# Optimization experiments

Hardware: AMD Instinct MI355X
Metric: run time of the kernel (lower is better)

## Reference

```python
import jax, jax.numpy as jnp
import numpy as np

MAX_TOP_K = 3
NUM_EXPERTS = 64
B, S, D = 4, 4096, 4096
H = D // 2


def setup_inputs() -> dict:
    key = jax.random.key(0)
    k0, k1, k2, k3 = jax.random.split(key, 4)
    x = jax.random.normal(k0, (B, S, D), dtype=jnp.float32)
    W = jax.random.normal(k1, (D, NUM_EXPERTS), dtype=jnp.float32) * 0.1
    # top_k_predictor: Linear(D, D//2) -> ReLU -> Linear(D//2, 1) -> Sigmoid
    W1 = jax.random.normal(k2, (D, H), dtype=jnp.float32) * (1.0 / np.sqrt(D))
    b1 = jnp.zeros((H,), dtype=jnp.float32)
    W2 = jax.random.normal(k3, (H, 1), dtype=jnp.float32) * (1.0 / np.sqrt(H))
    b2 = jnp.zeros((1,), dtype=jnp.float32)
    return {"x": x, "W": W, "W1": W1, "b1": b1, "W2": W2, "b2": b2}


def reference(x, W, W1, b1, W2, b2):
    b, s, d = x.shape
    x_flat = x.reshape(-1, d)                                  # [N, D]
    n = x_flat.shape[0]

    # small predictor MLP -> per-token dynamic k
    h = jax.nn.relu(x_flat @ W1 + b1)                          # [N, H]
    top_k_scores = jax.nn.sigmoid(h @ W2 + b2)[:, 0]           # [N]
    dynamic_top_k = jnp.clip(
        jnp.round(top_k_scores * MAX_TOP_K) + 1.0, 1.0, float(MAX_TOP_K)
    ).astype(jnp.int32)                                        # [N]

    # gating matmul + softmax + top-k
    gate_probs = jax.nn.softmax(x_flat @ W, axis=-1)           # [N, E]
    top_k_probs, top_k_indices = jax.lax.top_k(gate_probs, MAX_TOP_K)  # [N, K]

    # per-token dynamic-k mask and renormalize
    k_mask = jnp.arange(MAX_TOP_K)[None, :] < dynamic_top_k[:, None]   # [N, K]
    top_k_probs = top_k_probs * k_mask.astype(top_k_probs.dtype)
    top_k_weights = top_k_probs / (top_k_probs.sum(-1, keepdims=True) + 1e-8)

    # routing mask: 1 where expert is in top-k AND its (masked) weight > 0
    rows = jnp.arange(n)[:, None]                              # [N, 1]
    routing_mask = jnp.zeros((n, NUM_EXPERTS), top_k_weights.dtype).at[
        rows, top_k_indices
    ].set((top_k_weights > 0).astype(top_k_weights.dtype))     # [N, E]

    return (
        top_k_weights,
        top_k_indices,
        routing_mask.reshape(b, s, NUM_EXPERTS),
        dynamic_top_k,
    )
```

## Files before the change

### kernel.cpp

```cpp
#include <hip/hip_runtime.h>
#include <hip/hip_bf16.h>
#include <math.h>

#define DD   4096
#define HH   2048
#define NE   64
#define BK   32
#define NT   16
#define GM   32

typedef __attribute__((ext_vector_type(8))) short bf16x8;
typedef __attribute__((ext_vector_type(4))) float f32x4;

__device__ __forceinline__ void async16(void* lds, const void* g) {
    __builtin_amdgcn_global_load_lds(
        (const __attribute__((address_space(1))) unsigned int*)g,
        (__attribute__((address_space(3))) unsigned int*)lds, 16, 0, 0);
}

__device__ __forceinline__ void split2(float a, float b, unsigned& hi, unsigned& lo) {
    __hip_bfloat162 h = __float22bfloat162_rn(make_float2(a, b));
    float2 hf = __bfloat1622float2(h);
    __hip_bfloat162 l = __float22bfloat162_rn(make_float2(a - hf.x, b - hf.y));
    __builtin_memcpy(&hi, &h, 4);
    __builtin_memcpy(&lo, &l, 4);
}

__global__ __launch_bounds__(256) void split_xf(
    const float* __restrict__ x, uint4* __restrict__ xfh, uint4* __restrict__ xfl)
{
    const int t = threadIdx.x;
    const int mt = blockIdx.x >> 7;
    const int ks = blockIdx.x & 127;
#pragma unroll
    for (int s2 = 0; s2 < 2; ++s2) {
        int s = t + s2 * 256;
        int fb = s >> 6, ln = s & 63;
        int row = mt * 128 + fb * 16 + (ln & 15);
        int k   = ks * 32 + (ln >> 4) * 8;
        const float* g = x + (size_t)row * DD + k;
        float4 a = *(const float4*)g, b = *(const float4*)(g + 4);
        unsigned h0, l0, h1, l1, h2, l2, h3, l3;
        split2(a.x, a.y, h0, l0); split2(a.z, a.w, h1, l1);
        split2(b.x, b.y, h2, l2); split2(b.z, b.w, h3, l3);
        size_t idx = ((size_t)blockIdx.x * 8 + fb) * 64 + ln;
        xfh[idx] = make_uint4(h0, h1, h2, h3);
        xfl[idx] = make_uint4(l0, l1, l2, l3);
    }
}

__global__ __launch_bounds__(256) void split_w1t(
    const float* __restrict__ W1,
    unsigned short* __restrict__ th, unsigned short* __restrict__ tl)
{
    __shared__ float ts[32][33];
    const int n0 = blockIdx.x * 32, k0 = blockIdx.y * 32;
    const int t = threadIdx.x;
    {
        int r = t >> 3, c4 = (t & 7) * 4;
        float4 v = *(const float4*)&W1[(size_t)(k0 + r) * HH + n0 + c4];
        ts[r][c4] = v.x; ts[r][c4 + 1] = v.y; ts[r][c4 + 2] = v.z; ts[r][c4 + 3] = v.w;
    }
    __syncthreads();
    int n = t >> 3, kk = (t & 7) * 4;
    float f0 = ts[kk][n], f1 = ts[kk + 1][n], f2 = ts[kk + 2][n], f3 = ts[kk + 3][n];
    unsigned h0, l0, h1, l1;
    split2(f0, f1, h0, l0); split2(f2, f3, h1, l1);
    *(uint2*)&th[(size_t)(n0 + n) * DD + k0 + kk] = make_uint2(h0, h1);
    *(uint2*)&tl[(size_t)(n0 + n) * DD + k0 + kk] = make_uint2(l0, l1);
}

template<bool PRE_A>
__global__ __launch_bounds__(256, 3) void pred_mfma(
    const float* __restrict__ x,
    const unsigned short* __restrict__ xh, const unsigned short* __restrict__ xl,
    const unsigned short* __restrict__ w1th, const unsigned short* __restrict__ w1tl,
    const float* __restrict__ b1, const float* __restrict__ W2,
    double* __restrict__ pl)
{
    __shared__ __align__(16) char lds[32768];

    const int t = threadIdx.x, wv = t >> 6, ln = t & 63;
    const int lin = blockIdx.x;
    const int sub = lin >> 3;
    const int ntile = (lin & 7) * 2 + (sub & 1);
    const int mtile = sub >> 1;
    const int m0 = mtile * 128, n0 = ntile * 128;
    const int frow = ln & 15;
    const int fkb  = (ln >> 4) * 8;

    f32x4 acc[4][4];
#pragma unroll
    for (int i = 0; i < 4; ++i)
#pragma unroll
        for (int j = 0; j < 4; ++j) acc[i][j] = (f32x4){0.f, 0.f, 0.f, 0.f};

    const int mb = (wv & 1) * 4, nb = (wv >> 1) * 4;

    if (PRE_A) {
        const unsigned short* bsrc = (wv & 2) ? w1tl : w1th;
        const int roleoff = ((wv & 2) ? 8192 : 0) + (wv & 1) * 4096;
        const unsigned short* bg =
            bsrc + (size_t)(n0 + (wv & 1) * 64 + frow) * DD + fkb;

        const uint4* gh = (const uint4*)xh + ((size_t)mtile * 1024 + mb) * 64 + ln;
        const uint4* gl = (const uint4*)xl + ((size_t)mtile * 1024 + mb) * 64 + ln;

        bf16x8 ah[4], al[4];

#pragma unroll
        for (int q = 0; q < 4; ++q)
            async16(lds + roleoff + q * 1024, bg + (size_t)q * 16 * DD);
        __builtin_amdgcn_sched_barrier(0);
#pragma unroll
        for (int i = 0; i < 4; ++i) {
            ah[i] = *(const bf16x8*)(gh + i * 64);
            al[i] = *(const bf16x8*)(gl + i * 64);
        }
        asm volatile("s_waitcnt vmcnt(8)" ::: "memory");
        __builtin_amdgcn_s_barrier();

        for (int ks = 0; ks < 128; ++ks) {
            const int rb = (ks & 1) << 14;
            const int sb = rb ^ 16384;
            const bool more = (ks + 1 < 128);

            if (more) {
#pragma unroll
                for (int q = 0; q < 4; ++q)
                    async16(lds + sb + roleoff + q * 1024,
                            bg + (size_t)q * 16 * DD + (ks + 1) * BK);
            }
            __builtin_amdgcn_sched_barrier(0);

            bf16x8 bfh[4], bfl[4];
#pragma unroll
            for (int j = 0; j < 4; ++j) {
                bfh[j] = *(const bf16x8*)(lds + rb + (nb + j) * 1024 + ln * 16);
                bfl[j] = *(const bf16x8*)(lds + rb + 8192 + (nb + j) * 1024 + ln * 16);
            }

#pragma unroll
            for (int i = 0; i < 4; ++i)
#pragma unroll
                for (int j = 0; j < 4; ++j) {
                    acc[i][j] = __builtin_amdgcn_mfma_f32_16x16x32_bf16(ah[i], bfh[j], acc[i][j], 0, 0, 0);
                    acc[i][j] = __builtin_amdgcn_mfma_f32_16x16x32_bf16(ah[i], bfl[j], acc[i][j], 0, 0, 0);
                }
            if (more) {
#pragma unroll
                for (int i = 0; i < 4; ++i)
                    ah[i] = *(const bf16x8*)(gh + (size_t)(ks + 1) * 512 + i * 64);
            }
#pragma unroll
            for (int i = 0; i < 4; ++i)
#pragma unroll
                for (int j = 0; j < 4; ++j)
                    acc[i][j] = __builtin_amdgcn_mfma_f32_16x16x32_bf16(al[i], bfh[j], acc[i][j], 0, 0, 0);
            if (more) {
#pragma unroll
                for (int i = 0; i < 4; ++i)
                    al[i] = *(const bf16x8*)(gl + (size_t)(ks + 1) * 512 + i * 64);
                asm volatile("s_waitcnt vmcnt(8)" ::: "memory");
                __builtin_amdgcn_s_barrier();
            }
        }
    } else {
        char* Ah = lds;
        char* Al = lds + 8192;
        char* Bh = lds + 16384;
        char* Bl = lds + 24576;
        const unsigned short* gBh = w1th + (size_t)(n0 + frow) * DD + fkb;
        const unsigned short* gBl = w1tl + (size_t)(n0 + frow) * DD + fkb;

        for (int kc = 0; kc < DD; kc += BK) {
#pragma unroll
            for (int q = 0; q < 2; ++q) {
                int fb = wv * 2 + q;
                async16(Bh + fb * 1024, gBh + (size_t)fb * 16 * DD + kc);
                async16(Bl + fb * 1024, gBl + (size_t)fb * 16 * DD + kc);
            }
#pragma unroll
            for (int s2 = 0; s2 < 2; ++s2) {
                int s = t + s2 * 256;
                int fb = s >> 6, sl = s & 63;
                int row = fb * 16 + (sl & 15), kb = (sl >> 4) * 8;
                const float* g = x + (size_t)(m0 + row) * DD + kc + kb;
                float4 a = *(const float4*)g, b = *(const float4*)(g + 4);
                unsigned h0, l0, h1, l1, h2, l2, h3, l3;
                split2(a.x, a.y, h0, l0); split2(a.z, a.w, h1, l1);
                split2(b.x, b.y, h2, l2); split2(b.z, b.w, h3, l3);
                *(uint4*)(Ah + s * 16) = make_uint4(h0, h1, h2, h3);
                *(uint4*)(Al + s * 16) = make_uint4(l0, l1, l2, l3);
            }
            __syncthreads();

            bf16x8 afh[4], afl[4], bfh[4], bfl[4];
#pragma unroll
            for (int i = 0; i < 4; ++i) {
                afh[i] = *(const bf16x8*)(Ah + (mb + i) * 1024 + ln * 16);
                afl[i] = *(const bf16x8*)(Al + (mb + i) * 1024 + ln * 16);
                bfh[i] = *(const bf16x8*)(Bh + (nb + i) * 1024 + ln * 16);
                bfl[i] = *(const bf16x8*)(Bl + (nb + i) * 1024 + ln * 16);
            }
#pragma unroll
            for (int i = 0; i < 4; ++i)
#pragma unroll
                for (int j = 0; j < 4; ++j) {
                    acc[i][j] = __builtin_amdgcn_mfma_f32_16x16x32_bf16(afh[i], bfh[j], acc[i][j], 0, 0, 0);
                    acc[i][j] = __builtin_amdgcn_mfma_f32_16x16x32_bf16(afh[i], bfl[j], acc[i][j], 0, 0, 0);
                    acc[i][j] = __builtin_amdgcn_mfma_f32_16x16x32_bf16(afl[i], bfh[j], acc[i][j], 0, 0, 0);
                }
            __syncthreads();
        }
    }

    __syncthreads();
    double* redd = (double*)lds;
    const int mh = wv & 1, nh = wv >> 1;
    float b1v[4], w2v[4];
#pragma unroll
    for (int j = 0; j < 4; ++j) {
        int col = n0 + nh * 64 + j * 16 + frow;
        b1v[j] = b1[col];
        w2v[j] = W2[col];
    }
#pragma unroll
    for (int i = 0; i < 4; ++i)
#pragma unroll
        for (int r = 0; r < 4; ++r) {
            double s = 0.0;
#pragma unroll
            for (int j = 0; j < 4; ++j) {
                float h = acc[i][j][r] + b1v[j];
                h = fmaxf(h, 0.f);
                s += (double)h * (double)w2v[j];
            }
#pragma unroll
            for (int o = 1; o < 16; o <<= 1) s += __shfl_xor(s, o, 64);
            if (frow == 0)
                redd[nh * 128 + mh * 64 + i * 16 + (ln >> 4) * 4 + r] = s;
        }
    __syncthreads();
    if (t < 128)
        pl[(size_t)(m0 + t) * NT + ntile] = redd[t] + redd[128 + t];
}

__global__ __launch_bounds__(256) void pred_gemm(
    const float* __restrict__ x, const float* __restrict__ W1,
    const float* __restrict__ b1, const float* __restrict__ W2,
    double* __restrict__ pl)
{
    __shared__ float As[BK][128];
    __shared__ float Bs[BK][128];
    __shared__ double red[128][NT + 1];

    const int ht = blockIdx.x;
    const int tm = blockIdx.y;
    const int t  = threadIdx.x;
    const int tx = t & 15, ty = t >> 4;
    const int h0 = ht * 128;
    const int m0 = tm * 128;

    float acc[8][8];
#pragma unroll
    for (int i = 0; i < 8; ++i)
#pragma unroll
        for (int j = 0; j < 8; ++j) acc[i][j] = 0.f;

    const int arow = t >> 1, acol = (t & 1) << 4;
    const int brow = t >> 3, bcol = (t & 7) << 4;
    const float* xrow = x  + (size_t)(m0 + arow) * DD + acol;
    const float* wrow = W1 + (size_t)brow * HH + h0 + bcol;

    for (int k0 = 0; k0 < DD; k0 += BK) {
        float4 a4[4], b4[4];
        const float4* ap = (const float4*)(xrow + k0);
#pragma unroll
        for (int i = 0; i < 4; ++i) a4[i] = ap[i];
        const float4* bp = (const float4*)(wrow + (size_t)k0 * HH);
#pragma unroll
        for (int i = 0; i < 4; ++i) b4[i] = bp[i];
        __syncthreads();
#pragma unroll
        for (int i = 0; i < 4; ++i) {
            As[acol + i * 4 + 0][arow] = a4[i].x;
            As[acol + i * 4 + 1][arow] = a4[i].y;
            As[acol + i * 4 + 2][arow] = a4[i].z;
            As[acol + i * 4 + 3][arow] = a4[i].w;
        }
#pragma unroll
        for (int i = 0; i < 4; ++i)
            *(float4*)&Bs[brow][bcol + i * 4] = b4[i];
        __syncthreads();
#pragma unroll 8
        for (int kk = 0; kk < BK; ++kk) {
            float4 a0  = *(const float4*)&As[kk][ty * 8];
            float4 a1  = *(const float4*)&As[kk][ty * 8 + 4];
            float4 bb0 = *(const float4*)&Bs[kk][tx * 8];
            float4 bb1 = *(const float4*)&Bs[kk][tx * 8 + 4];
            float av[8] = {a0.x, a0.y, a0.z, a0.w, a1.x, a1.y, a1.z, a1.w};
            float bv[8] = {bb0.x, bb0.y, bb0.z, bb0.w, bb1.x, bb1.y, bb1.z, bb1.w};
#pragma unroll
            for (int i = 0; i < 8; ++i)
#pragma unroll
                for (int j = 0; j < 8; ++j)
                    acc[i][j] = fmaf(av[i], bv[j], acc[i][j]);
        }
    }
    __syncthreads();
#pragma unroll
    for (int r = 0; r < 8; ++r) {
        double s = 0.0;
#pragma unroll
        for (int c = 0; c < 8; ++c) {
            int h = h0 + tx * 8 + c;
            float v = acc[r][c] + b1[h];
            v = v > 0.f ? v : 0.f;
            s += (double)v * (double)W2[h];
        }
        red[ty * 8 + r][tx] = s;
    }
    __syncthreads();
    if (t < 128) {
        double s = 0.0;
#pragma unroll
        for (int j = 0; j < NT; ++j) s += red[t][j];
        pl[(size_t)(m0 + t) * NT + ht] = s;
    }
}

__global__ __launch_bounds__(256) void gate_fused(
    const float* __restrict__ x, const float* __restrict__ W,
    const double* __restrict__ pl, const float* __restrict__ b2,
    float* __restrict__ out, int Ntok)
{
    __shared__ __align__(16) char smem[GM * (NE + 1) * sizeof(double)];
    float (*As)[GM] = (float(*)[GM])smem;
    float (*Bs)[NE] = (float(*)[NE])(smem + BK * GM * 4);
    double (*Dm)[NE + 1] = (double(*)[NE + 1])smem;

    const int tm = blockIdx.x;
    const int t  = threadIdx.x;
    const int tx = t & 15, ty = t >> 4;
    const int m0 = tm * GM;

    double acc[2][4];
#pragma unroll
    for (int i = 0; i < 2; ++i)
#pragma unroll
        for (int j = 0; j < 4; ++j) acc[i][j] = 0.0;

    const int arow = t >> 3, acol = (t & 7) * 4;
    const int brow = t >> 3, bcol = (t & 7) * 8;
    const float* xrow = x + (size_t)(m0 + arow) * DD + acol;
    const float* wrow = W + (size_t)brow * NE + bcol;

    float4 a4  = *(const float4*)xrow;
    float4 b40 = *(const float4*)wrow;
    float4 b41 = *(const float4*)(wrow + 4);

    for (int k0 = 0; k0 < DD; k0 += BK) {
        __syncthreads();
        As[acol + 0][arow] = a4.x;
        As[acol + 1][arow] = a4.y;
        As[acol + 2][arow] = a4.z;
        As[acol + 3][arow] = a4.w;
        *(float4*)&Bs[brow][bcol]     = b40;
        *(float4*)&Bs[brow][bcol + 4] = b41;
        __syncthreads();

        if (k0 + BK < DD) {
            a4  = *(const float4*)(xrow + k0 + BK);
            b40 = *(const float4*)(wrow + (size_t)(k0 + BK) * NE);
            b41 = *(const float4*)(wrow + (size_t)(k0 + BK) * NE + 4);
        }

#pragma unroll 8
        for (int kk = 0; kk < BK; ++kk) {
            double a0 = (double)As[kk][ty * 2];
            double a1 = (double)As[kk][ty * 2 + 1];
            float4 b = *(const float4*)&Bs[kk][tx * 4];
            double bv[4] = {(double)b.x, (double)b.y, (double)b.z, (double)b.w};
#pragma unroll
            for (int j = 0; j < 4; ++j) {
                acc[0][j] = fma(a0, bv[j], acc[0][j]);
                acc[1][j] = fma(a1, bv[j], acc[1][j]);
            }
        }
    }

    __syncthreads();
#pragma unroll
    for (int r = 0; r < 2; ++r)
#pragma unroll
        for (int c = 0; c < 4; ++c)
            Dm[ty * 2 + r][tx * 4 + c] = acc[r][c];
    __syncthreads();

    const int wave = t >> 6;
    const int lane = t & 63;
    const double b2v = (double)b2[0];

    for (int i = 0; i < 8; ++i) {
        const int tl = wave * 8 + i;
        const int token = m0 + tl;
        double g = Dm[tl][lane];

        double mx = g;
#pragma unroll
        for (int o = 32; o > 0; o >>= 1) mx = fmax(mx, __shfl_xor(mx, o, 64));
        double e = exp(g - mx);
        double s = e;
#pragma unroll
        for (int o = 32; o > 0; o >>= 1) s += __shfl_xor(s, o, 64);
        double p = e / s;

        double pv = p; int pi = lane;
        double vt[3]; int it[3];
#pragma unroll
        for (int j = 0; j < 3; ++j) {
            double v = pv; int idx = pi;
#pragma unroll
            for (int o = 32; o > 0; o >>= 1) {
                double ov = __shfl_xor(v, o, 64);
                int    oi = __shfl_xor(idx, o, 64);
                if (ov > v || (ov == v && oi < idx)) { v = ov; idx = oi; }
            }
            vt[j] = v; it[j] = idx;
            if (lane == idx) pv = -1.0;
        }

        double plv = (lane < NT) ? pl[(size_t)token * NT + lane] : 0.0;
#pragma unroll
        for (int o = 32; o > 0; o >>= 1) plv += __shfl_xor(plv, o, 64);
        double logit = plv + b2v;
        double score = 1.0 / (1.0 + exp(-logit));
        int k = (int)rint(score * 3.0) + 1;
        k = k < 1 ? 1 : (k > 3 ? 3 : k);

        double wmask[3]; double wsum = 0.0;
#pragma unroll
        for (int j = 0; j < 3; ++j) { wmask[j] = (j < k) ? vt[j] : 0.0; wsum += wmask[j]; }
        double denom = wsum + 1e-8;
        float wn[3];
#pragma unroll
        for (int j = 0; j < 3; ++j) wn[j] = (float)(wmask[j] / denom);

        float mval = 0.f;
#pragma unroll
        for (int j = 0; j < 3; ++j)
            if (it[j] == lane && wn[j] > 0.f) mval = 1.f;

        out[(size_t)6 * Ntok + (size_t)token * NE + lane] = mval;
        if (lane < 3) {
            out[(size_t)token * 3 + lane] = wn[lane];
            out[(size_t)3 * Ntok + (size_t)token * 3 + lane] = (float)it[lane];
        }
        if (lane == 0) out[(size_t)70 * Ntok + token] = (float)k;
    }
}

extern "C" void kernel_launch(void* const* d_in, const int* in_sizes, int n_in,
                              void* d_out, int out_size, void* d_ws, size_t ws_size,
                              hipStream_t stream)
{
    const float* x  = (const float*)d_in[0];
    const float* W  = (const float*)d_in[1];
    const float* W1 = (const float*)d_in[2];
    const float* b1 = (const float*)d_in[3];
    const float* W2 = (const float*)d_in[4];
    const float* b2 = (const float*)d_in[5];
    float* out = (float*)d_out;

    const int Ntok = in_sizes[0] / DD;

    double* pl = (double*)d_ws;
    const size_t pl_b   = (size_t)Ntok * NT * sizeof(double);
    const size_t o_w1h  = (pl_b + 255) & ~(size_t)255;
    const size_t w1_b   = (size_t)DD * HH * 2;
    const size_t o_w1l  = o_w1h + w1_b;
    const size_t o_xh   = o_w1l + w1_b;
    const size_t x_b    = (size_t)Ntok * DD * 2;
    const size_t o_xl   = o_xh + x_b;
    const size_t need_w1   = o_xh;
    const size_t need_full = o_xl + x_b;

    const bool ok128 = (Ntok % 128) == 0;

    if (ok128 && ws_size >= need_w1) {
        unsigned short* w1th = (unsigned short*)((char*)d_ws + o_w1h);
        unsigned short* w1tl = (unsigned short*)((char*)d_ws + o_w1l);
        split_w1t<<<dim3(HH / 32, DD / 32), 256, 0, stream>>>(W1, w1th, w1tl);
        if (ws_size >= need_full) {
            unsigned short* xfh = (unsigned short*)((char*)d_ws + o_xh);
            unsigned short* xfl = (unsigned short*)((char*)d_ws + o_xl);
            split_xf<<<Ntok, 256, 0, stream>>>(x, (uint4*)xfh, (uint4*)xfl);
            pred_mfma<true><<<16 * (Ntok / 128), 256, 0, stream>>>(
                x, xfh, xfl, w1th, w1tl, b1, W2, pl);
        } else {
            pred_mfma<false><<<16 * (Ntok / 128), 256, 0, stream>>>(
                x, nullptr, nullptr, w1th, w1tl, b1, W2, pl);
        }
    } else {
        pred_gemm<<<dim3(NT, Ntok / 128), 256, 0, stream>>>(x, W1, b1, W2, pl);
    }

    gate_fused<<<Ntok / GM, 256, 0, stream>>>(x, W, pl, b2, out, Ntok);
}
```

Measured before the change: 1.549 ms.

## Repartition MFMA warp tiling to 32x128 per wave and drop LDS reduction

Each wave now owns 2 row fragments across all 8 column fragments (32x128) instead of a 4x4 fragment block. Every wave therefore reads all B fragments from LDS and holds half as many A fragments in registers fetched straight from global memory. With full columns per wave, the partial dot with W2 is complete within a wave and is written directly to the output, removing the LDS reduction and the final barrier. The fallback path that split x inside the kernel is deleted, so the MFMA path now needs the full workspace. The trade is twice the LDS B reads per wave and uneven register pressure.

```diff
diff --git a/kernel.cpp b/kernel.cpp
--- a/kernel.cpp
+++ b/kernel.cpp
@@ -70,9 +70,7 @@
     *(uint2*)&tl[(size_t)(n0 + n) * DD + k0 + kk] = make_uint2(l0, l1);
 }
 
-template<bool PRE_A>
 __global__ __launch_bounds__(256, 3) void pred_mfma(
-    const float* __restrict__ x,
     const unsigned short* __restrict__ xh, const unsigned short* __restrict__ xl,
     const unsigned short* __restrict__ w1th, const unsigned short* __restrict__ w1tl,
     const float* __restrict__ b1, const float* __restrict__ W2,
@@ -89,161 +87,128 @@
     const int frow = ln & 15;
     const int fkb  = (ln >> 4) * 8;
 
-    f32x4 acc[4][4];
-#pragma unroll
-    for (int i = 0; i < 4; ++i)
-#pragma unroll
-        for (int j = 0; j < 4; ++j) acc[i][j] = (f32x4){0.f, 0.f, 0.f, 0.f};
-
-    const int mb = (wv & 1) * 4, nb = (wv >> 1) * 4;
-
-    if (PRE_A) {
-        const unsigned short* bsrc = (wv & 2) ? w1tl : w1th;
-        const int roleoff = ((wv & 2) ? 8192 : 0) + (wv & 1) * 4096;
-        const unsigned short* bg =
-            bsrc + (size_t)(n0 + (wv & 1) * 64 + frow) * DD + fkb;
-
-        const uint4* gh = (const uint4*)xh + ((size_t)mtile * 1024 + mb) * 64 + ln;
-        const uint4* gl = (const uint4*)xl + ((size_t)mtile * 1024 + mb) * 64 + ln;
-
-        bf16x8 ah[4], al[4];
-
-#pragma unroll
-        for (int q = 0; q < 4; ++q)
-            async16(lds + roleoff + q * 1024, bg + (size_t)q * 16 * DD);
+    f32x4 acc[2][8];
+#pragma unroll
+    for (int i = 0; i < 2; ++i)
+#pragma unroll
+        for (int j = 0; j < 8; ++j) acc[i][j] = (f32x4){0.f, 0.f, 0.f, 0.f};
+
+    const unsigned short* bsrc = (wv & 2) ? w1tl : w1th;
+    const int roleoff = ((wv & 2) ? 8192 : 0) + (wv & 1) * 4096;
+    const unsigned short* bg =
+        bsrc + (size_t)(n0 + (wv & 1) * 64 + frow) * DD + fkb;
+
+    const uint4* gh = (const uint4*)xh + ((size_t)mtile * 1024 + wv * 2) * 64 + ln;
+    const uint4* gl = (const uint4*)xl + ((size_t)mtile * 1024 + wv * 2) * 64 + ln;
+
+    bf16x8 ah[2], al[2];
+
+#pragma unroll
+    for (int q = 0; q < 4; ++q)
+        async16(lds + roleoff + q * 1024, bg + (size_t)q * 16 * DD);
+    __builtin_amdgcn_sched_barrier(0);
+#pragma unroll
+    for (int i = 0; i < 2; ++i) {
+        ah[i] = *(const bf16x8*)(gh + i * 64);
+        al[i] = *(const bf16x8*)(gl + i * 64);
+    }
+    asm volatile("s_waitcnt vmcnt(4)" ::: "memory");
+    __builtin_amdgcn_s_barrier();
+
+    for (int ks = 0; ks < 128; ++ks) {
+        const int rb = (ks & 1) << 14;
+        const int sb = rb ^ 16384;
+        const bool more = (ks + 1 < 128);
+
+        if (more) {
+#pragma unroll
+            for (int q = 0; q < 4; ++q)
+                async16(lds + sb + roleoff + q * 1024,
+                        bg + (size_t)q * 16 * DD + (ks + 1) * BK);
+        }
         __builtin_amdgcn_sched_barrier(0);
-#pragma unroll
-        for (int i = 0; i < 4; ++i) {
-            ah[i] = *(const bf16x8*)(gh + i * 64);
-            al[i] = *(const bf16x8*)(gl + i * 64);
-        }
-        asm volatile("s_waitcnt vmcnt(8)" ::: "memory");
-        __builtin_amdgcn_s_barrier();
-
-        for (int ks = 0; ks < 128; ++ks) {
-            const int rb = (ks & 1) << 14;
-            const int sb = rb ^ 16384;
-            const bool more = (ks + 1 < 128);
-
-            if (more) {
-#pragma unroll
-                for (int q = 0; q < 4; ++q)
-                    async16(lds + sb + roleoff + q * 1024,
-                            bg + (size_t)q * 16 * DD + (ks + 1) * BK);
-            }
-            __builtin_amdgcn_sched_barrier(0);
-
+
+        {
             bf16x8 bfh[4], bfl[4];
 #pragma unroll
             for (int j = 0; j < 4; ++j) {
-                bfh[j] = *(const bf16x8*)(lds + rb + (nb + j) * 1024 + ln * 16);
-                bfl[j] = *(const bf16x8*)(lds + rb + 8192 + (nb + j) * 1024 + ln * 16);
-            }
-
-#pragma unroll
-            for (int i = 0; i < 4; ++i)
+                bfh[j] = *(const bf16x8*)(lds + rb + j * 1024 + ln * 16);
+                bfl[j] = *(const bf16x8*)(lds + rb + 8192 + j * 1024 + ln * 16);
+            }
+#pragma unroll
+            for (int i = 0; i < 2; ++i)
 #pragma unroll
                 for (int j = 0; j < 4; ++j) {
                     acc[i][j] = __builtin_amdgcn_mfma_f32_16x16x32_bf16(ah[i], bfh[j], acc[i][j], 0, 0, 0);
                     acc[i][j] = __builtin_amdgcn_mfma_f32_16x16x32_bf16(ah[i], bfl[j], acc[i][j], 0, 0, 0);
                 }
-            if (more) {
-#pragma unroll
-                for (int i = 0; i < 4; ++i)
-                    ah[i] = *(const bf16x8*)(gh + (size_t)(ks + 1) * 512 + i * 64);
-            }
-#pragma unroll
-            for (int i = 0; i < 4; ++i)
+#pragma unroll
+            for (int i = 0; i < 2; ++i)
 #pragma unroll
                 for (int j = 0; j < 4; ++j)
                     acc[i][j] = __builtin_amdgcn_mfma_f32_16x16x32_bf16(al[i], bfh[j], acc[i][j], 0, 0, 0);
+        }
+
+        {
+            bf16x8 bfh[4], bfl[4];
+#pragma unroll
+            for (int j = 0; j < 4; ++j) {
+                bfh[j] = *(const bf16x8*)(lds + rb + (4 + j) * 1024 + ln * 16);
+                bfl[j] = *(const bf16x8*)(lds + rb + 8192 + (4 + j) * 1024 + ln * 16);
+            }
+#pragma unroll
+            for (int i = 0; i < 2; ++i)
+#pragma unroll
+                for (int j = 0; j < 4; ++j) {
+                    acc[i][4 + j] = __builtin_amdgcn_mfma_f32_16x16x32_bf16(ah[i], bfh[j], acc[i][4 + j], 0, 0, 0);
+                    acc[i][4 + j] = __builtin_amdgcn_mfma_f32_16x16x32_bf16(ah[i], bfl[j], acc[i][4 + j], 0, 0, 0);
+                }
             if (more) {
 #pragma unroll
-                for (int i = 0; i < 4; ++i)
-                    al[i] = *(const bf16x8*)(gl + (size_t)(ks + 1) * 512 + i * 64);
-                asm volatile("s_waitcnt vmcnt(8)" ::: "memory");
-                __builtin_amdgcn_s_barrier();
-            }
-        }
-    } else {
-        char* Ah = lds;
-        char* Al = lds + 8192;
-        char* Bh = lds + 16384;
-        char* Bl = lds + 24576;
-        const unsigned short* gBh = w1th + (size_t)(n0 + frow) * DD + fkb;
-        const unsigned short* gBl = w1tl + (size_t)(n0 + frow) * DD + fkb;
-
-        for (int kc = 0; kc < DD; kc += BK) {
-#pragma unroll
-            for (int q = 0; q < 2; ++q) {
-                int fb = wv * 2 + q;
-                async16(Bh + fb * 1024, gBh + (size_t)fb * 16 * DD + kc);
-                async16(Bl + fb * 1024, gBl + (size_t)fb * 16 * DD + kc);
-            }
-#pragma unroll
-            for (int s2 = 0; s2 < 2; ++s2) {
-                int s = t + s2 * 256;
-                int fb = s >> 6, sl = s & 63;
-                int row = fb * 16 + (sl & 15), kb = (sl >> 4) * 8;
-                const float* g = x + (size_t)(m0 + row) * DD + kc + kb;
-                float4 a = *(const float4*)g, b = *(const float4*)(g + 4);
-                unsigned h0, l0, h1, l1, h2, l2, h3, l3;
-                split2(a.x, a.y, h0, l0); split2(a.z, a.w, h1, l1);
-                split2(b.x, b.y, h2, l2); split2(b.z, b.w, h3, l3);
-                *(uint4*)(Ah + s * 16) = make_uint4(h0, h1, h2, h3);
-                *(uint4*)(Al + s * 16) = make_uint4(l0, l1, l2, l3);
-            }
-            __syncthreads();
-
-            bf16x8 afh[4], afl[4], bfh[4], bfl[4];
-#pragma unroll
-            for (int i = 0; i < 4; ++i) {
-                afh[i] = *(const bf16x8*)(Ah + (mb + i) * 1024 + ln * 16);
-                afl[i] = *(const bf16x8*)(Al + (mb + i) * 1024 + ln * 16);
-                bfh[i] = *(const bf16x8*)(Bh + (nb + i) * 1024 + ln * 16);
-                bfl[i] = *(const bf16x8*)(Bl + (nb + i) * 1024 + ln * 16);
-            }
-#pragma unroll
-            for (int i = 0; i < 4; ++i)
-#pragma unroll
-                for (int j = 0; j < 4; ++j) {
-                    acc[i][j] = __builtin_amdgcn_mfma_f32_16x16x32_bf16(afh[i], bfh[j], acc[i][j], 0, 0, 0);
-                    acc[i][j] = __builtin_amdgcn_mfma_f32_16x16x32_bf16(afh[i], bfl[j], acc[i][j], 0, 0, 0);
-                    acc[i][j] = __builtin_amdgcn_mfma_f32_16x16x32_bf16(afl[i], bfh[j], acc[i][j], 0, 0, 0);
-                }
-            __syncthreads();
-        }
-    }
-
-    __syncthreads();
-    double* redd = (double*)lds;
-    const int mh = wv & 1, nh = wv >> 1;
-    float b1v[4], w2v[4];
-#pragma unroll
-    for (int j = 0; j < 4; ++j) {
-        int col = n0 + nh * 64 + j * 16 + frow;
+                for (int i = 0; i < 2; ++i)
+                    ah[i] = *(const bf16x8*)(gh + (size_t)(ks + 1) * 512 + i * 64);
+            }
+#pragma unroll
+            for (int i = 0; i < 2; ++i)
+#pragma unroll
+                for (int j = 0; j < 4; ++j)
+                    acc[i][4 + j] = __builtin_amdgcn_mfma_f32_16x16x32_bf16(al[i], bfh[j], acc[i][4 + j], 0, 0, 0);
+        }
+
+        if (more) {
+#pragma unroll
+            for (int i = 0; i < 2; ++i)
+                al[i] = *(const bf16x8*)(gl + (size_t)(ks + 1) * 512 + i * 64);
+            asm volatile("s_waitcnt vmcnt(4)" ::: "memory");
+            __builtin_amdgcn_s_barrier();
+        }
+    }
+
+    float b1v[8], w2v[8];
+#pragma unroll
+    for (int j = 0; j < 8; ++j) {
+        int col = n0 + j * 16 + frow;
         b1v[j] = b1[col];
         w2v[j] = W2[col];
     }
 #pragma unroll
-    for (int i = 0; i < 4; ++i)
+    for (int i = 0; i < 2; ++i)
 #pragma unroll
         for (int r = 0; r < 4; ++r) {
             double s = 0.0;
 #pragma unroll
-            for (int j = 0; j < 4; ++j) {
+            for (int j = 0; j < 8; ++j) {
                 float h = acc[i][j][r] + b1v[j];
                 h = fmaxf(h, 0.f);
                 s += (double)h * (double)w2v[j];
             }
 #pragma unroll
             for (int o = 1; o < 16; o <<= 1) s += __shfl_xor(s, o, 64);
-            if (frow == 0)
-                redd[nh * 128 + mh * 64 + i * 16 + (ln >> 4) * 4 + r] = s;
-        }
-    __syncthreads();
-    if (t < 128)
-        pl[(size_t)(m0 + t) * NT + ntile] = redd[t] + redd[128 + t];
+            if (frow == 0) {
+                int row = m0 + (wv * 2 + i) * 16 + (ln >> 4) * 4 + r;
+                pl[(size_t)row * NT + ntile] = s;
+            }
+        }
 }
 
 __global__ __launch_bounds__(256) void pred_gemm(
@@ -483,25 +448,19 @@
     const size_t o_xh   = o_w1l + w1_b;
     const size_t x_b    = (size_t)Ntok * DD * 2;
     const size_t o_xl   = o_xh + x_b;
-    const size_t need_w1   = o_xh;
     const size_t need_full = o_xl + x_b;
 
     const bool ok128 = (Ntok % 128) == 0;
 
-    if (ok128 && ws_size >= need_w1) {
+    if (ok128 && ws_size >= need_full) {
         unsigned short* w1th = (unsigned short*)((char*)d_ws + o_w1h);
         unsigned short* w1tl = (unsigned short*)((char*)d_ws + o_w1l);
+        unsigned short* xfh  = (unsigned short*)((char*)d_ws + o_xh);
+        unsigned short* xfl  = (unsigned short*)((char*)d_ws + o_xl);
         split_w1t<<<dim3(HH / 32, DD / 32), 256, 0, stream>>>(W1, w1th, w1tl);
-        if (ws_size >= need_full) {
-            unsigned short* xfh = (unsigned short*)((char*)d_ws + o_xh);
-            unsigned short* xfl = (unsigned short*)((char*)d_ws + o_xl);
-            split_xf<<<Ntok, 256, 0, stream>>>(x, (uint4*)xfh, (uint4*)xfl);
-            pred_mfma<true><<<16 * (Ntok / 128), 256, 0, stream>>>(
-                x, xfh, xfl, w1th, w1tl, b1, W2, pl);
-        } else {
-            pred_mfma<false><<<16 * (Ntok / 128), 256, 0, stream>>>(
-                x, nullptr, nullptr, w1th, w1tl, b1, W2, pl);
-        }
+        split_xf<<<Ntok, 256, 0, stream>>>(x, (uint4*)xfh, (uint4*)xfl);
+        pred_mfma<<<16 * (Ntok / 128), 256, 0, stream>>>(
+            xfh, xfl, w1th, w1tl, b1, W2, pl);
     } else {
         pred_gemm<<<dim3(NT, Ntok / 128), 256, 0, stream>>>(x, W1, b1, W2, pl);
     }
```

New measurement: 1.477 ms. -4.6%, faster.
